# Performance work log

Measured on AMD Instinct MI355X. Metric: run time of the kernel, lower is better.

The kernel has to match this reference:

```python
import jax, jax.numpy as jnp
import numpy as np

DIM, ORDER, HID = 512, 2, 64
B, S = 4, 8192


def setup_inputs() -> dict:
    key = jax.random.key(0)
    ks = jax.random.split(key, 16)
    rnd = lambda k, shape, scale: (jax.random.normal(k, shape, dtype=jnp.float32) * scale)
    return {
        'x': rnd(ks[0], (B, S, DIM), 1.0),
        # ImplicitFilter MLP: Linear(1,64) -> GELU -> Linear(64,64) -> GELU -> Linear(64,dim)
        'w1': rnd(ks[1], (1, HID), 1.0),
        'b1': rnd(ks[2], (HID,), 0.02),
        'w2': rnd(ks[3], (HID, HID), 1.0 / np.sqrt(HID)),
        'b2': rnd(ks[4], (HID,), 0.02),
        'w3': rnd(ks[5], (HID, DIM), 1.0 / np.sqrt(HID)),
        'b3': rnd(ks[6], (DIM,), 0.02),
        # depthwise Conv1d(dim, dim, k=3, padding=1, groups=dim): weight (dim, 3)
        'conv_w': rnd(ks[7], (DIM, 3), 1.0 / np.sqrt(3)),
        'conv_b': rnd(ks[8], (DIM,), 0.02),
        # in_proj: Linear(dim, dim*(order+1))
        'w_in': rnd(ks[9], (DIM, DIM * (ORDER + 1)), 1.0 / np.sqrt(DIM)),
        'b_in': rnd(ks[10], (DIM * (ORDER + 1),), 0.02),
        # out_proj: Linear(dim, dim)
        'w_out': rnd(ks[11], (DIM, DIM), 1.0 / np.sqrt(DIM)),
        'b_out': rnd(ks[12], (DIM,), 0.02),
    }


def _gelu(x):
    return jax.nn.gelu(x, approximate=False)  # torch nn.GELU default is exact erf


def reference(x, w1, b1, w2, b2, w3, b3, conv_w, conv_b, w_in, b_in, w_out, b_out):
    batch, seq_len, dim = x.shape
    # in_proj and split into order+1 paths
    proj = x @ w_in + b_in                      # (B, S, 3D)
    v, u, z = jnp.split(proj, 3, axis=-1)       # each (B, S, D)
    # implicit filter from positions
    pos = jnp.linspace(0.0, 1.0, seq_len, dtype=x.dtype)[:, None]   # (S, 1)
    filt = _gelu(_gelu(pos @ w1 + b1) @ w2 + b2) @ w3 + b3          # (S, D)
    # depthwise short conv, kernel=3, padding=1 (cross-correlation as in torch)
    up = jnp.pad(u, ((0, 0), (1, 1), (0, 0)))
    u_short = (up[:, :-2] * conv_w[:, 0] + up[:, 1:-1] * conv_w[:, 1]
               + up[:, 2:] * conv_w[:, 2] + conv_b)                 # (B, S, D)
    # FFT long convolution (circular, matching torch rfft/irfft with n=seq_len)
    U = jnp.fft.rfft(u_short, axis=1)                               # (B, S//2+1, D)
    F = jnp.fft.rfft(filt, n=seq_len, axis=0)[None]                 # (1, S//2+1, D)
    filtered = jnp.fft.irfft(U * F, n=seq_len, axis=1)              # (B, S, D)
    # multiplicative gates
    out = v * filtered * jax.nn.sigmoid(z)
    return out @ w_out + b_out
```

## Files before the change

### kernel.cpp

```cpp
#include <hip/hip_runtime.h>
#include <math.h>

#define DIM   512
#define NB    4
#define NS    8192
#define FFT_N 8192
#define FT    1024
#define MTOT  (NB*NS)

#define IDX(i) ((i) + ((i) >> 3))
#define XSZ   9216

typedef __attribute__((ext_vector_type(8))) short bf16x8;
typedef __attribute__((ext_vector_type(4))) short short4v;
typedef __attribute__((ext_vector_type(8))) short short8v;
typedef __attribute__((ext_vector_type(4))) float f32x4;

__device__ __forceinline__ float bf2f(unsigned short u) {
    union { unsigned int i; float f; } v; v.i = ((unsigned int)u) << 16; return v.f;
}
__device__ __forceinline__ unsigned short f2bf(float f) {
    union { float f; unsigned int i; } v; v.f = f;
    unsigned int r = v.i + 0x7fffu + ((v.i >> 16) & 1u);
    return (unsigned short)(r >> 16);
}
__device__ __forceinline__ float2 cmulf(float2 a, float2 b) {
    return make_float2(a.x*b.x - a.y*b.y, a.x*b.y + a.y*b.x);
}
__device__ __forceinline__ float2 cadd(float2 a, float2 b) { return make_float2(a.x+b.x, a.y+b.y); }
__device__ __forceinline__ float2 csub(float2 a, float2 b) { return make_float2(a.x-b.x, a.y-b.y); }
__device__ __forceinline__ float gelu_exact(float x) {
    return 0.5f * x * (1.0f + erff(x * 0.70710678118654752f));
}
__device__ __forceinline__ void gload16(const void* g, void* l) {
    __builtin_amdgcn_global_load_lds((const __attribute__((address_space(1))) void*)g,
                                     (__attribute__((address_space(3))) void*)l, 16, 0, 0);
}

__device__ __forceinline__ void castT_body(const float* __restrict__ in,
                                           unsigned short* __restrict__ outT,
                                           int R, int C, int bx, int by, int t,
                                           float tile[64][65]) {
    const int c0 = bx * 64, r0 = by * 64;
    const int rr = t >> 4, c4 = (t & 15) * 4;
    #pragma unroll
    for (int p = 0; p < 4; ++p) {
        const int r = rr + p*16;
        float4 v = *(const float4*)&in[(size_t)(r0 + r)*C + c0 + c4];
        tile[r][c4+0]=v.x; tile[r][c4+1]=v.y; tile[r][c4+2]=v.z; tile[r][c4+3]=v.w;
    }
    __syncthreads();
    const int cc = t >> 4, r4 = (t & 15) * 4;
    #pragma unroll
    for (int p = 0; p < 4; ++p) {
        const int c = cc + p*16;
        short4v o;
        o[0] = (short)f2bf(tile[r4+0][c]); o[1] = (short)f2bf(tile[r4+1][c]);
        o[2] = (short)f2bf(tile[r4+2][c]); o[3] = (short)f2bf(tile[r4+3][c]);
        *(short4v*)&outT[(size_t)(c0 + c)*R + r0 + r4] = o;
    }
}

__global__ void mega_prep_kernel(const float* __restrict__ x, unsigned short* __restrict__ xb,
                                 const float* __restrict__ w_in, unsigned short* __restrict__ w_inT,
                                 const float* __restrict__ w_out, unsigned short* __restrict__ w_outT,
                                 const float* __restrict__ w1, const float* __restrict__ b1,
                                 const float* __restrict__ w2, const float* __restrict__ b2,
                                 const float* __restrict__ w3, const float* __restrict__ b3,
                                 float* __restrict__ filt) {
    __shared__ float tile[64][65];
    __shared__ float h1s[4][64];
    __shared__ float h2s[4][64];
    const int bid = blockIdx.x;
    const int t = threadIdx.x;
    if (bid < 8192) {
        const size_t i = ((size_t)bid * 256 + t) * 8;
        float4 a = *(const float4*)&x[i];
        float4 b = *(const float4*)&x[i+4];
        short8v o;
        o[0]=(short)f2bf(a.x); o[1]=(short)f2bf(a.y); o[2]=(short)f2bf(a.z); o[3]=(short)f2bf(a.w);
        o[4]=(short)f2bf(b.x); o[5]=(short)f2bf(b.y); o[6]=(short)f2bf(b.z); o[7]=(short)f2bf(b.w);
        *(short8v*)&xb[i] = o;
    } else if (bid < 8384) {
        const int li = bid - 8192;
        castT_body(w_in, w_inT, DIM, 1536, li % 24, li / 24, t, tile);
    } else if (bid < 8448) {
        const int li = bid - 8384;
        castT_body(w_out, w_outT, DIM, DIM, li % 8, li / 8, t, tile);
    } else {
        const int sub = t >> 6, lane = t & 63;
        const int s = (bid - 8448) * 4 + sub;
        const float pos = (float)s / (float)(NS - 1);
        h1s[sub][lane] = gelu_exact(pos * w1[lane] + b1[lane]);
        __syncthreads();
        float acc = b2[lane];
        #pragma unroll 8
        for (int j = 0; j < 64; ++j) acc += h1s[sub][j] * w2[j*64 + lane];
        h2s[sub][lane] = gelu_exact(acc);
        __syncthreads();
        for (int d = lane; d < DIM; d += 64) {
            float o = b3[d];
            #pragma unroll 8
            for (int j = 0; j < 64; ++j) o += h2s[sub][j] * w3[j*DIM + d];
            filt[(size_t)s*DIM + d] = o;
        }
    }
}

template<int LOGQ>
__device__ __forceinline__ void dif4_stage(float2* X) {
    const int q = 1 << LOGQ;
    const float step = -6.28318530717958647692f / (float)(4*q);
    #pragma unroll
    for (int it = 0; it < (FFT_N/4)/FT; ++it) {
        const int idx = threadIdx.x + it*FT;
        const int g = idx >> LOGQ, k = idx & (q-1);
        const int base = (g << (LOGQ+2)) + k;
        const int i0 = IDX(base), i1 = IDX(base+q), i2 = IDX(base+2*q), i3 = IDX(base+3*q);
        float2 a=X[i0], b=X[i1], c=X[i2], d=X[i3];
        float2 t0=cadd(a,c), t1=csub(a,c), t2=cadd(b,d), t3=csub(b,d);
        float2 y0=cadd(t0,t2), y2=csub(t0,t2);
        float2 y1=make_float2(t1.x+t3.y, t1.y-t3.x);
        float2 y3=make_float2(t1.x-t3.y, t1.y+t3.x);
        float sv, cv; __sincosf(step*(float)k, &sv, &cv);
        float2 w1=make_float2(cv, sv);
        float2 w2=cmulf(w1, w1);
        float2 w3=cmulf(w2, w1);
        X[i0] = y0;
        X[i1] = cmulf(y1, w1);
        X[i2] = cmulf(y2, w2);
        X[i3] = cmulf(y3, w3);
    }
    __syncthreads();
}

template<int LOGQ>
__device__ __forceinline__ void dit4_stage_inv(float2* X) {
    const int q = 1 << LOGQ;
    const float step = 6.28318530717958647692f / (float)(4*q);
    #pragma unroll
    for (int it = 0; it < (FFT_N/4)/FT; ++it) {
        const int idx = threadIdx.x + it*FT;
        const int g = idx >> LOGQ, k = idx & (q-1);
        const int base = (g << (LOGQ+2)) + k;
        const int i0 = IDX(base), i1 = IDX(base+q), i2 = IDX(base+2*q), i3 = IDX(base+3*q);
        float sv, cv; __sincosf(step*(float)k, &sv, &cv);
        float2 w1=make_float2(cv, sv);
        float2 w2=cmulf(w1, w1);
        float2 w3=cmulf(w2, w1);
        float2 u0=X[i0];
        float2 u1=cmulf(X[i1], w1);
        float2 u2=cmulf(X[i2], w2);
        float2 u3=cmulf(X[i3], w3);
        float2 s02=cadd(u0,u2), d02=csub(u0,u2);
        float2 s13=cadd(u1,u3), d13=csub(u1,u3);
        X[i0] = cadd(s02, s13);
        X[i2] = csub(s02, s13);
        X[i1] = make_float2(d02.x - d13.y, d02.y + d13.x);
        X[i3] = make_float2(d02.x + d13.y, d02.y - d13.x);
    }
    __syncthreads();
}

__device__ __forceinline__ void reg_fwd(float2* E) {
    const float C = 0.70710678118654752f;
    {
        float2 t0=cadd(E[0],E[4]), t1=csub(E[0],E[4]);
        float2 t2=cadd(E[2],E[6]), t3=csub(E[2],E[6]);
        E[0]=cadd(t0,t2);
        E[4]=csub(t0,t2);
        E[2]=make_float2(t1.x+t3.y, t1.y-t3.x);
        E[6]=make_float2(t1.x-t3.y, t1.y+t3.x);
    }
    {
        float2 t0=cadd(E[1],E[5]), t1=csub(E[1],E[5]);
        float2 t2=cadd(E[3],E[7]), t3=csub(E[3],E[7]);
        float2 y0=cadd(t0,t2), y2=csub(t0,t2);
        float2 y1=make_float2(t1.x+t3.y, t1.y-t3.x);
        float2 y3=make_float2(t1.x-t3.y, t1.y+t3.x);
        E[1]=y0;
        E[3]=make_float2(C*(y1.x+y1.y),  C*(y1.y-y1.x));
        E[5]=make_float2(y2.y, -y2.x);
        E[7]=make_float2(C*(y3.y-y3.x), -C*(y3.x+y3.y));
    }
    #pragma unroll
    for (int j = 0; j < 8; j += 2) {
        float2 a=E[j], b=E[j+1];
        E[j]=cadd(a,b); E[j+1]=csub(a,b);
    }
}
__device__ __forceinline__ void reg_inv(float2* E) {
    const float C = 0.70710678118654752f;
    #pragma unroll
    for (int j = 0; j < 8; j += 2) {
        float2 a=E[j], b=E[j+1];
        E[j]=cadd(a,b); E[j+1]=csub(a,b);
    }
    {
        float2 u0=E[0], u1=E[2], u2=E[4], u3=E[6];
        float2 s02=cadd(u0,u2), d02=csub(u0,u2);
        float2 s13=cadd(u1,u3), d13=csub(u1,u3);
        E[0]=cadd(s02,s13);
        E[4]=csub(s02,s13);
        E[2]=make_float2(d02.x - d13.y, d02.y + d13.x);
        E[6]=make_float2(d02.x + d13.y, d02.y - d13.x);
    }
    {
        float2 z1=E[3], z2=E[5], z3=E[7];
        float2 u0=E[1];
        float2 u1=make_float2(C*(z1.x - z1.y), C*(z1.x + z1.y));
        float2 u2=make_float2(-z2.y, z2.x);
        float2 u3=make_float2(-C*(z3.x + z3.y), C*(z3.x - z3.y));
        float2 s02=cadd(u0,u2), d02=csub(u0,u2);
        float2 s13=cadd(u1,u3), d13=csub(u1,u3);
        E[1]=cadd(s02,s13);
        E[5]=csub(s02,s13);
        E[3]=make_float2(d02.x - d13.y, d02.y + d13.x);
        E[7]=make_float2(d02.x + d13.y, d02.y - d13.x);
    }
}

__device__ __forceinline__ void load8p(const float2* X, int t, float2* E) {
    const float2* b = X + 9*t;
    #pragma unroll
    for (int j = 0; j < 8; ++j) E[j] = b[j];
}
__device__ __forceinline__ void store8p(float2* X, int t, const float2* E) {
    float2* b = X + 9*t;
    #pragma unroll
    for (int j = 0; j < 8; ++j) b[j] = E[j];
}

__global__ __launch_bounds__(FT)
void filtconv_kernel(const float* __restrict__ filtT, float2* __restrict__ Fbr,
                     const unsigned short* __restrict__ u,
                     const float* __restrict__ conv_w, const float* __restrict__ conv_b,
                     unsigned short* __restrict__ uT) {
    __shared__ __align__(16) char fsm[XSZ * sizeof(float2)];
    const int bid = blockIdx.x;
    const int t = threadIdx.x;
    if (bid < 512) {
        float2* X = (float2*)fsm;
        const int dd = bid;
        const float* f = filtT + (size_t)dd * FFT_N;
        {
            float4 a = *(const float4*)(f + 8*t);
            float4 b = *(const float4*)(f + 8*t + 4);
            float2 E[8];
            E[0]=make_float2(a.x,0.f); E[1]=make_float2(a.y,0.f);
            E[2]=make_float2(a.z,0.f); E[3]=make_float2(a.w,0.f);
            E[4]=make_float2(b.x,0.f); E[5]=make_float2(b.y,0.f);
            E[6]=make_float2(b.z,0.f); E[7]=make_float2(b.w,0.f);
            store8p(X, t, E);
        }
        __syncthreads();
        dif4_stage<11>(X);
        dif4_stage<9>(X);
        dif4_stage<7>(X);
        dif4_stage<5>(X);
        dif4_stage<3>(X);
        {
            float2 E[8];
            load8p(X, t, E);
            reg_fwd(E);
            float2* o = Fbr + (size_t)dd*FFT_N + 8*t;
            #pragma unroll
            for (int j = 0; j < 8; ++j) o[j] = E[j];
        }
    } else {
        float (*tile)[65] = (float(*)[65])fsm;
        const int lb = bid - 512;
        const int dt = lb & 7, st = (lb >> 3) & 127, b = lb >> 10;
        const int d0 = dt*64, s0 = st*64;
        const int rr = t >> 4, c4 = (t & 15) * 4;
        for (int r = rr; r < 66; r += 64) {
            const int s = s0 + r - 1;
            float v0=0.f, v1=0.f, v2=0.f, v3=0.f;
            if (s >= 0 && s < NS) {
                short4v xv = *(const short4v*)&u[((size_t)(b*NS + s))*DIM + d0 + c4];
                v0=bf2f((unsigned short)xv[0]); v1=bf2f((unsigned short)xv[1]);
                v2=bf2f((unsigned short)xv[2]); v3=bf2f((unsigned short)xv[3]);
            }
            tile[r][c4]=v0; tile[r][c4+1]=v1; tile[r][c4+2]=v2; tile[r][c4+3]=v3;
        }
        __syncthreads();
        const int dc = t >> 4, s4 = (t & 15) * 4;
        const int d = d0 + dc;
        const float w0 = conv_w[d*3], w1 = conv_w[d*3+1], w2 = conv_w[d*3+2];
        const float cb = conv_b[d];
        short4v o;
        #pragma unroll
        for (int j = 0; j < 4; ++j) {
            const int sx = s4 + j;
            const float val = tile[sx][dc]*w0 + tile[sx+1][dc]*w1 + tile[sx+2][dc]*w2 + cb;
            o[j] = (short)f2bf(val);
        }
        *(short4v*)&uT[((size_t)(b*DIM + d))*FFT_N + s0 + s4] = o;
    }
}

__global__ __launch_bounds__(FT)
void fft_conv_kernel(unsigned short* __restrict__ uT, const float2* __restrict__ Fbr) {
    __shared__ float2 X[XSZ];
    const int d = blockIdx.x & (DIM - 1);
    const int p = blockIdx.x >> 9;
    unsigned short* u1 = uT + (size_t)((2*p    )*DIM + d) * FFT_N;
    unsigned short* u2 = uT + (size_t)((2*p + 1)*DIM + d) * FFT_N;
    const int t = threadIdx.x;
    {
        short8v a = *(const short8v*)(u1 + 8*t);
        short8v b = *(const short8v*)(u2 + 8*t);
        float2 E[8];
        #pragma unroll
        for (int j = 0; j < 8; ++j)
            E[j] = make_float2(bf2f((unsigned short)a[j]), bf2f((unsigned short)b[j]));
        store8p(X, t, E);
    }
    __syncthreads();
    dif4_stage<11>(X);
    dif4_stage<9>(X);
    dif4_stage<7>(X);
    dif4_stage<5>(X);
    dif4_stage<3>(X);
    {
        float2 E[8];
        load8p(X, t, E);
        reg_fwd(E);
        const float2* F = Fbr + (size_t)d*FFT_N + 8*t;
        #pragma unroll
        for (int j = 0; j < 8; ++j) E[j] = cmulf(E[j], F[j]);
        reg_inv(E);
        store8p(X, t, E);
    }
    __syncthreads();
    dit4_stage_inv<3>(X);
    dit4_stage_inv<5>(X);
    dit4_stage_inv<7>(X);
    dit4_stage_inv<9>(X);
    dit4_stage_inv<11>(X);
    {
        float2 E[8];
        load8p(X, t, E);
        const float sc = 1.0f / (float)FFT_N;
        short8v a, b;
        #pragma unroll
        for (int j = 0; j < 8; ++j) {
            a[j] = (short)f2bf(E[j].x * sc);
            b[j] = (short)f2bf(E[j].y * sc);
        }
        *(short8v*)(u1 + 8*t) = a;
        *(short8v*)(u2 + 8*t) = b;
    }
}

__global__ void gate_kernel(unsigned short* __restrict__ vg, const unsigned short* __restrict__ yT) {
    __shared__ float tile[64][65];
    const int bid = blockIdx.x;
    const int dt = bid & 7, st = (bid >> 3) & 127, b = bid >> 10;
    const int d0 = dt*64, s0 = st*64;
    const int t = threadIdx.x;
    const int dl = t >> 4, s4 = (t & 15) * 4;
    #pragma unroll
    for (int p = 0; p < 4; ++p) {
        const int d = dl + p*16;
        short4v y = *(const short4v*)&yT[((size_t)(b*DIM + d0 + d))*FFT_N + s0 + s4];
        tile[d][s4]  =bf2f((unsigned short)y[0]); tile[d][s4+1]=bf2f((unsigned short)y[1]);
        tile[d][s4+2]=bf2f((unsigned short)y[2]); tile[d][s4+3]=bf2f((unsigned short)y[3]);
    }
    __syncthreads();
    const int sl = t >> 4, d4 = (t & 15) * 4;
    #pragma unroll
    for (int p = 0; p < 4; ++p) {
        const int s = s0 + sl + p*16;
        unsigned short* pv = &vg[((size_t)(b*NS + s))*DIM + d0 + d4];
        short4v v = *(short4v*)pv;
        short4v o;
        #pragma unroll
        for (int j = 0; j < 4; ++j)
            o[j] = (short)f2bf(bf2f((unsigned short)v[j]) * tile[d4+j][sl + p*16]);
        *(short4v*)pv = o;
    }
}

template<int MODE>
__global__ __launch_bounds__(256)
void gemm_bt_kernel(const unsigned short* __restrict__ A,
                    const unsigned short* __restrict__ BT,
                    const float* __restrict__ bias,
                    float* __restrict__ Cf,
                    unsigned short* __restrict__ Cb) {
    __shared__ unsigned short As[2][4096];
    __shared__ unsigned short Bs[2][4096];
    const int tid = threadIdx.x;
    const int wid = tid >> 6, lane = tid & 63;
    const int bid = blockIdx.y * 4 + blockIdx.x;
    const int swz = (bid & 7) * 128 + (bid >> 3);
    const int m0 = (swz >> 2) * 128, n0 = (swz & 3) * 128;
    const int srow = wid*16 + (lane >> 2);
    const int scol = (lane & 3) * 8;
    const unsigned short* gA = A  + (size_t)(m0 + srow)*DIM + scol;
    const unsigned short* gB = BT + (size_t)(n0 + srow)*DIM + scol;
    const int wr = wid >> 1, wc = wid & 1;
    const int fr = lane & 15, fq = lane >> 4;
    f32x4 acc[4][4] = {};
    gload16(gA,                  &As[0][wid*512]);
    gload16(gA + (size_t)64*DIM, &As[0][wid*512 + 2048]);
    gload16(gB,                  &Bs[0][wid*512]);
    gload16(gB + (size_t)64*DIM, &Bs[0][wid*512 + 2048]);
    int cur = 0;
    for (int k0 = 0; k0 < DIM; k0 += 32) {
        __syncthreads();
        if (k0 + 32 < DIM) {
            const int nx = cur ^ 1;
            gload16(gA + k0 + 32,                  &As[nx][wid*512]);
            gload16(gA + k0 + 32 + (size_t)64*DIM, &As[nx][wid*512 + 2048]);
            gload16(gB + k0 + 32,                  &Bs[nx][wid*512]);
            gload16(gB + k0 + 32 + (size_t)64*DIM, &Bs[nx][wid*512 + 2048]);
        }
        bf16x8 af[4], bfr[4];
        #pragma unroll
        for (int mi = 0; mi < 4; ++mi)
            af[mi] = *(const bf16x8*)&As[cur][(wr*64 + mi*16 + fr)*32 + fq*8];
        #pragma unroll
        for (int ni = 0; ni < 4; ++ni)
            bfr[ni] = *(const bf16x8*)&Bs[cur][(wc*64 + ni*16 + fr)*32 + fq*8];
        #pragma unroll
        for (int mi = 0; mi < 4; ++mi)
            #pragma unroll
            for (int ni = 0; ni < 4; ++ni)
                acc[mi][ni] = __builtin_amdgcn_mfma_f32_16x16x32_bf16(af[mi], bfr[ni], acc[mi][ni], 0, 0, 0);
        cur ^= 1;
    }
    #pragma unroll
    for (int ni = 0; ni < 4; ++ni) {
        const int c = n0 + wc*64 + ni*16 + fr;
        const float bv = bias[c];
        #pragma unroll
        for (int mi = 0; mi < 4; ++mi) {
            const int rbase = m0 + wr*64 + mi*16 + fq*4;
            #pragma unroll
            for (int j = 0; j < 4; ++j) {
                const size_t idx = (size_t)(rbase + j)*DIM + c;
                const float val = acc[mi][ni][j] + bv;
                if (MODE == 0) Cb[idx] = f2bf(val);
                else           Cf[idx] = val;
            }
        }
    }
}

__global__ __launch_bounds__(256)
void gemm_vzu2t_kernel(const unsigned short* __restrict__ A,
                       const unsigned short* __restrict__ BT,
                       const float* __restrict__ bias,
                       unsigned short* __restrict__ Gb,
                       unsigned short* __restrict__ Ub,
                       const float* __restrict__ filt,
                       float* __restrict__ filtT) {
    __shared__ __align__(16) char gsm[49152];
    unsigned short (*As)[4096] = (unsigned short(*)[4096])(gsm);
    unsigned short (*B1)[4096] = (unsigned short(*)[4096])(gsm + 16384);
    unsigned short (*B2)[4096] = (unsigned short(*)[4096])(gsm + 32768);
    const int tid = threadIdx.x;
    const int wid = tid >> 6, lane = tid & 63;
    const int bid = blockIdx.y * 4 + blockIdx.x;

    if (bid >= 2048) {
        float (*tile)[65] = (float(*)[65])gsm;
        const int li = bid - 2048;
        const int c0 = (li & 7) * 64, r0 = (li >> 3) * 64;
        const int rr = tid >> 4, c4 = (tid & 15) * 4;
        #pragma unroll
        for (int p = 0; p < 4; ++p) {
            const int r = rr + p*16;
            float4 v = *(const float4*)&filt[(size_t)(r0 + r)*DIM + c0 + c4];
            tile[r][c4+0]=v.x; tile[r][c4+1]=v.y; tile[r][c4+2]=v.z; tile[r][c4+3]=v.w;
        }
        __syncthreads();
        const int cc = tid >> 4, r4 = (tid & 15) * 4;
        #pragma unroll
        for (int p = 0; p < 4; ++p) {
            const int c = cc + p*16;
            float4 o = make_float4(tile[r4+0][c], tile[r4+1][c], tile[r4+2][c], tile[r4+3][c]);
            *(float4*)&filtT[(size_t)(c0 + c)*NS + r0 + r4] = o;
        }
        return;
    }

    const bool is_u = bid >= 1024;
    const int lbid = bid & 1023;
    const int swz = (lbid & 7) * 128 + (lbid >> 3);
    const int m0 = (swz >> 2) * 128, n0 = (swz & 3) * 128;
    const int srow = wid*16 + (lane >> 2);
    const int scol = (lane & 3) * 8;
    const unsigned short* gA = A + (size_t)(m0 + srow)*DIM + scol;
    const int wr = wid >> 1, wc = wid & 1;
    const int fr = lane & 15, fq = lane >> 4;

    if (!is_u) {
        const unsigned short* gBv = BT + (size_t)(n0 + srow)*DIM + scol;
        const unsigned short* gBz = BT + (size_t)(1024 + n0 + srow)*DIM + scol;
        f32x4 accv[4][4] = {};
        f32x4 accz[4][4] = {};
        gload16(gA,                   &As[0][wid*512]);
        gload16(gA  + (size_t)64*DIM, &As[0][wid*512 + 2048]);
        gload16(gBv,                  &B1[0][wid*512]);
        gload16(gBv + (size_t)64*DIM, &B1[0][wid*512 + 2048]);
        gload16(gBz,                  &B2[0][wid*512]);
        gload16(gBz + (size_t)64*DIM, &B2[0][wid*512 + 2048]);
        int cur = 0;
        for (int k0 = 0; k0 < DIM; k0 += 32) {
            __syncthreads();
            if (k0 + 32 < DIM) {
                const int nx = cur ^ 1;
                gload16(gA  + k0 + 32,                  &As[nx][wid*512]);
                gload16(gA  + k0 + 32 + (size_t)64*DIM, &As[nx][wid*512 + 2048]);
                gload16(gBv + k0 + 32,                  &B1[nx][wid*512]);
                gload16(gBv + k0 + 32 + (size_t)64*DIM, &B1[nx][wid*512 + 2048]);
                gload16(gBz + k0 + 32,                  &B2[nx][wid*512]);
                gload16(gBz + k0 + 32 + (size_t)64*DIM, &B2[nx][wid*512 + 2048]);
            }
            bf16x8 af[4], bf_[4];
            #pragma unroll
            for (int mi = 0; mi < 4; ++mi)
                af[mi] = *(const bf16x8*)&As[cur][(wr*64 + mi*16 + fr)*32 + fq*8];
            #pragma unroll
            for (int ni = 0; ni < 4; ++ni)
                bf_[ni] = *(const bf16x8*)&B1[cur][(wc*64 + ni*16 + fr)*32 + fq*8];
            #pragma unroll
            for (int mi = 0; mi < 4; ++mi)
                #pragma unroll
                for (int ni = 0; ni < 4; ++ni)
                    accv[mi][ni] = __builtin_amdgcn_mfma_f32_16x16x32_bf16(af[mi], bf_[ni], accv[mi][ni], 0, 0, 0);
            #pragma unroll
            for (int ni = 0; ni < 4; ++ni)
                bf_[ni] = *(const bf16x8*)&B2[cur][(wc*64 + ni*16 + fr)*32 + fq*8];
            #pragma unroll
            for (int mi = 0; mi < 4; ++mi)
                #pragma unroll
                for (int ni = 0; ni < 4; ++ni)
                    accz[mi][ni] = __builtin_amdgcn_mfma_f32_16x16x32_bf16(af[mi], bf_[ni], accz[mi][ni], 0, 0, 0);
            cur ^= 1;
        }
        #pragma unroll
        for (int ni = 0; ni < 4; ++ni) {
            const int c = n0 + wc*64 + ni*16 + fr;
            const float bv = bias[c];
            const float bz = bias[1024 + c];
            #pragma unroll
            for (int mi = 0; mi < 4; ++mi) {
                const int rbase = m0 + wr*64 + mi*16 + fq*4;
                #pragma unroll
                for (int j = 0; j < 4; ++j) {
                    const size_t idx = (size_t)(rbase + j)*DIM + c;
                    const float vv = accv[mi][ni][j] + bv;
                    const float zz = accz[mi][ni][j] + bz;
                    const float sg = 1.0f / (1.0f + __expf(-zz));
                    Gb[idx] = f2bf(vv * sg);
                }
            }
        }
    } else {
        const unsigned short* gBu = BT + (size_t)(512 + n0 + srow)*DIM + scol;
        f32x4 acc[4][4] = {};
        gload16(gA,                   &As[0][wid*512]);
        gload16(gA  + (size_t)64*DIM, &As[0][wid*512 + 2048]);
        gload16(gBu,                  &B1[0][wid*512]);
        gload16(gBu + (size_t)64*DIM, &B1[0][wid*512 + 2048]);
        int cur = 0;
        for (int k0 = 0; k0 < DIM; k0 += 32) {
            __syncthreads();
            if (k0 + 32 < DIM) {
                const int nx = cur ^ 1;
                gload16(gA  + k0 + 32,                  &As[nx][wid*512]);
                gload16(gA  + k0 + 32 + (size_t)64*DIM, &As[nx][wid*512 + 2048]);
                gload16(gBu + k0 + 32,                  &B1[nx][wid*512]);
                gload16(gBu + k0 + 32 + (size_t)64*DIM, &B1[nx][wid*512 + 2048]);
            }
            bf16x8 af[4], bf_[4];
            #pragma unroll
            for (int mi = 0; mi < 4; ++mi)
                af[mi] = *(const bf16x8*)&As[cur][(wr*64 + mi*16 + fr)*32 + fq*8];
            #pragma unroll
            for (int ni = 0; ni < 4; ++ni)
                bf_[ni] = *(const bf16x8*)&B1[cur][(wc*64 + ni*16 + fr)*32 + fq*8];
            #pragma unroll
            for (int mi = 0; mi < 4; ++mi)
                #pragma unroll
                for (int ni = 0; ni < 4; ++ni)
                    acc[mi][ni] = __builtin_amdgcn_mfma_f32_16x16x32_bf16(af[mi], bf_[ni], acc[mi][ni], 0, 0, 0);
            cur ^= 1;
        }
        #pragma unroll
        for (int ni = 0; ni < 4; ++ni) {
            const int c = n0 + wc*64 + ni*16 + fr;
            const float bu = bias[512 + c];
            #pragma unroll
            for (int mi = 0; mi < 4; ++mi) {
                const int rbase = m0 + wr*64 + mi*16 + fq*4;
                #pragma unroll
                for (int j = 0; j < 4; ++j) {
                    const size_t idx = (size_t)(rbase + j)*DIM + c;
                    Ub[idx] = f2bf(acc[mi][ni][j] + bu);
                }
            }
        }
    }
}

extern "C" void kernel_launch(void* const* d_in, const int* in_sizes, int n_in,
                              void* d_out, int out_size, void* d_ws, size_t ws_size,
                              hipStream_t stream) {
    const float* x      = (const float*)d_in[0];
    const float* w1     = (const float*)d_in[1];
    const float* b1     = (const float*)d_in[2];
    const float* w2     = (const float*)d_in[3];
    const float* b2     = (const float*)d_in[4];
    const float* w3     = (const float*)d_in[5];
    const float* b3     = (const float*)d_in[6];
    const float* conv_w = (const float*)d_in[7];
    const float* conv_b = (const float*)d_in[8];
    const float* w_in   = (const float*)d_in[9];
    const float* b_in   = (const float*)d_in[10];
    const float* w_out  = (const float*)d_in[11];
    const float* b_out  = (const float*)d_in[12];
    float* out = (float*)d_out;

    const size_t NEED = 167772160ULL;
    if (ws_size < NEED) return;
    char* ws = (char*)d_ws;
    float2*         Fbr    = (float2*)ws;
    float*          filt   = (float*)ws;
    unsigned short* xb     = (unsigned short*)(ws + (size_t)( 32<<20));
    unsigned short* W2     = (unsigned short*)(ws + (size_t)( 64<<20));
    unsigned short* W3     = (unsigned short*)(ws + (size_t)( 96<<20));
    char*           W4     = ws + (size_t)(128<<20);
    unsigned short* w_inT  = (unsigned short*)W4;
    unsigned short* w_outT = (unsigned short*)(W4 + (size_t)(2<<20));
    float*          filtT  = (float*)(W4 + (size_t)(4<<20));

    mega_prep_kernel<<<10496, 256, 0, stream>>>(x, xb, w_in, w_inT, w_out, w_outT,
                                                w1, b1, w2, b2, w3, b3, filt);
    gemm_vzu2t_kernel<<<dim3(4, 768), 256, 0, stream>>>(xb, w_inT, b_in, W2, W3, filt, filtT);
    filtconv_kernel<<<4608, FT, 0, stream>>>(filtT, Fbr, W3, conv_w, conv_b, xb);
    fft_conv_kernel<<<(NB/2)*DIM, FT, 0, stream>>>(xb, Fbr);
    gate_kernel<<<NB*(NS/64)*(DIM/64), 256, 0, stream>>>(W2, xb);
    gemm_bt_kernel<2><<<dim3(4, MTOT/128), 256, 0, stream>>>(W2, w_outT, b_out, out, nullptr);
}
```

Before: 257.4 us.

## Write u transposed from GEMM epilogue and fuse short conv into FFT load

The u-projection GEMM epilogue now stages its tile in shared memory and writes u directly in a (batch, dim, seq) transposed layout. The depthwise kernel-3 short convolution moves into the FFT kernel's load phase, using neighbour loads at the 8-element chunk edges. This drops the separate transpose-plus-conv pass and one full round trip of u through global memory. In exchange the GEMM epilogue gains two barriers and an LDS transpose, and the FFT kernel issues extra scalar halo loads.

Measured after the change: 247.0 us. 1.04x faster.

```diff
diff --git a/kernel.cpp b/kernel.cpp
--- a/kernel.cpp
+++ b/kernel.cpp
@@ -232,75 +232,40 @@
 }
 
 __global__ __launch_bounds__(FT)
-void filtconv_kernel(const float* __restrict__ filtT, float2* __restrict__ Fbr,
-                     const unsigned short* __restrict__ u,
-                     const float* __restrict__ conv_w, const float* __restrict__ conv_b,
-                     unsigned short* __restrict__ uT) {
-    __shared__ __align__(16) char fsm[XSZ * sizeof(float2)];
-    const int bid = blockIdx.x;
+void fft_filt_kernel(const float* __restrict__ filtT, float2* __restrict__ Fbr) {
+    __shared__ float2 X[XSZ];
+    const int dd = blockIdx.x;
     const int t = threadIdx.x;
-    if (bid < 512) {
-        float2* X = (float2*)fsm;
-        const int dd = bid;
-        const float* f = filtT + (size_t)dd * FFT_N;
-        {
-            float4 a = *(const float4*)(f + 8*t);
-            float4 b = *(const float4*)(f + 8*t + 4);
-            float2 E[8];
-            E[0]=make_float2(a.x,0.f); E[1]=make_float2(a.y,0.f);
-            E[2]=make_float2(a.z,0.f); E[3]=make_float2(a.w,0.f);
-            E[4]=make_float2(b.x,0.f); E[5]=make_float2(b.y,0.f);
-            E[6]=make_float2(b.z,0.f); E[7]=make_float2(b.w,0.f);
-            store8p(X, t, E);
-        }
-        __syncthreads();
-        dif4_stage<11>(X);
-        dif4_stage<9>(X);
-        dif4_stage<7>(X);
-        dif4_stage<5>(X);
-        dif4_stage<3>(X);
-        {
-            float2 E[8];
-            load8p(X, t, E);
-            reg_fwd(E);
-            float2* o = Fbr + (size_t)dd*FFT_N + 8*t;
-            #pragma unroll
-            for (int j = 0; j < 8; ++j) o[j] = E[j];
-        }
-    } else {
-        float (*tile)[65] = (float(*)[65])fsm;
-        const int lb = bid - 512;
-        const int dt = lb & 7, st = (lb >> 3) & 127, b = lb >> 10;
-        const int d0 = dt*64, s0 = st*64;
-        const int rr = t >> 4, c4 = (t & 15) * 4;
-        for (int r = rr; r < 66; r += 64) {
-            const int s = s0 + r - 1;
-            float v0=0.f, v1=0.f, v2=0.f, v3=0.f;
-            if (s >= 0 && s < NS) {
-                short4v xv = *(const short4v*)&u[((size_t)(b*NS + s))*DIM + d0 + c4];
-                v0=bf2f((unsigned short)xv[0]); v1=bf2f((unsigned short)xv[1]);
-                v2=bf2f((unsigned short)xv[2]); v3=bf2f((unsigned short)xv[3]);
-            }
-            tile[r][c4]=v0; tile[r][c4+1]=v1; tile[r][c4+2]=v2; tile[r][c4+3]=v3;
-        }
-        __syncthreads();
-        const int dc = t >> 4, s4 = (t & 15) * 4;
-        const int d = d0 + dc;
-        const float w0 = conv_w[d*3], w1 = conv_w[d*3+1], w2 = conv_w[d*3+2];
-        const float cb = conv_b[d];
-        short4v o;
-        #pragma unroll
-        for (int j = 0; j < 4; ++j) {
-            const int sx = s4 + j;
-            const float val = tile[sx][dc]*w0 + tile[sx+1][dc]*w1 + tile[sx+2][dc]*w2 + cb;
-            o[j] = (short)f2bf(val);
-        }
-        *(short4v*)&uT[((size_t)(b*DIM + d))*FFT_N + s0 + s4] = o;
+    const float* f = filtT + (size_t)dd * FFT_N;
+    {
+        float4 a = *(const float4*)(f + 8*t);
+        float4 b = *(const float4*)(f + 8*t + 4);
+        float2 E[8];
+        E[0]=make_float2(a.x,0.f); E[1]=make_float2(a.y,0.f);
+        E[2]=make_float2(a.z,0.f); E[3]=make_float2(a.w,0.f);
+        E[4]=make_float2(b.x,0.f); E[5]=make_float2(b.y,0.f);
+        E[6]=make_float2(b.z,0.f); E[7]=make_float2(b.w,0.f);
+        store8p(X, t, E);
+    }
+    __syncthreads();
+    dif4_stage<11>(X);
+    dif4_stage<9>(X);
+    dif4_stage<7>(X);
+    dif4_stage<5>(X);
+    dif4_stage<3>(X);
+    {
+        float2 E[8];
+        load8p(X, t, E);
+        reg_fwd(E);
+        float2* o = Fbr + (size_t)dd*FFT_N + 8*t;
+        #pragma unroll
+        for (int j = 0; j < 8; ++j) o[j] = E[j];
     }
 }
 
 __global__ __launch_bounds__(FT)
-void fft_conv_kernel(unsigned short* __restrict__ uT, const float2* __restrict__ Fbr) {
+void fft_conv_kernel(unsigned short* __restrict__ uT, const float2* __restrict__ Fbr,
+                     const float* __restrict__ conv_w, const float* __restrict__ conv_b) {
     __shared__ float2 X[XSZ];
     const int d = blockIdx.x & (DIM - 1);
     const int p = blockIdx.x >> 9;
@@ -310,10 +275,25 @@
     {
         short8v a = *(const short8v*)(u1 + 8*t);
         short8v b = *(const short8v*)(u2 + 8*t);
+        const float al = (t == 0)    ? 0.f : bf2f(u1[8*t - 1]);
+        const float ar = (t == FT-1) ? 0.f : bf2f(u1[8*t + 8]);
+        const float bl = (t == 0)    ? 0.f : bf2f(u2[8*t - 1]);
+        const float br = (t == FT-1) ? 0.f : bf2f(u2[8*t + 8]);
+        const float w0 = conv_w[d*3], w1 = conv_w[d*3+1], w2c = conv_w[d*3+2];
+        const float cb = conv_b[d];
+        float xa[10], xb[10];
+        xa[0] = al; xb[0] = bl;
+        #pragma unroll
+        for (int j = 0; j < 8; ++j) {
+            xa[j+1] = bf2f((unsigned short)a[j]);
+            xb[j+1] = bf2f((unsigned short)b[j]);
+        }
+        xa[9] = ar; xb[9] = br;
         float2 E[8];
         #pragma unroll
         for (int j = 0; j < 8; ++j)
-            E[j] = make_float2(bf2f((unsigned short)a[j]), bf2f((unsigned short)b[j]));
+            E[j] = make_float2(w0*xa[j] + w1*xa[j+1] + w2c*xa[j+2] + cb,
+                               w0*xb[j] + w1*xb[j+1] + w2c*xb[j+2] + cb);
         store8p(X, t, E);
     }
     __syncthreads();
@@ -454,7 +434,7 @@
                        const unsigned short* __restrict__ BT,
                        const float* __restrict__ bias,
                        unsigned short* __restrict__ Gb,
-                       unsigned short* __restrict__ Ub,
+                       unsigned short* __restrict__ UbT,
                        const float* __restrict__ filt,
                        float* __restrict__ filtT) {
     __shared__ __align__(16) char gsm[49152];
@@ -591,20 +571,30 @@
                     acc[mi][ni] = __builtin_amdgcn_mfma_f32_16x16x32_bf16(af[mi], bf_[ni], acc[mi][ni], 0, 0, 0);
             cur ^= 1;
         }
+        __syncthreads();
+        unsigned short (*tileT)[136] = (unsigned short(*)[136])gsm;
         #pragma unroll
         for (int ni = 0; ni < 4; ++ni) {
-            const int c = n0 + wc*64 + ni*16 + fr;
-            const float bu = bias[512 + c];
+            const int dl = wc*64 + ni*16 + fr;
+            const float bu = bias[512 + n0 + dl];
             #pragma unroll
             for (int mi = 0; mi < 4; ++mi) {
-                const int rbase = m0 + wr*64 + mi*16 + fq*4;
+                const int slb = wr*64 + mi*16 + fq*4;
                 #pragma unroll
-                for (int j = 0; j < 4; ++j) {
-                    const size_t idx = (size_t)(rbase + j)*DIM + c;
-                    Ub[idx] = f2bf(acc[mi][ni][j] + bu);
-                }
+                for (int j = 0; j < 4; ++j)
+                    tileT[dl][slb + j] = f2bf(acc[mi][ni][j] + bu);
             }
         }
+        __syncthreads();
+        const int b   = m0 >> 13;
+        const int s0m = m0 & (NS - 1);
+        const int row  = tid >> 1;
+        const int half = (tid & 1) * 64;
+        unsigned short* dst = UbT + ((size_t)(b*DIM + n0 + row))*NS + s0m + half;
+        const unsigned short* srcT = &tileT[row][half];
+        #pragma unroll
+        for (int i = 0; i < 8; ++i)
+            *(short8v*)(dst + i*8) = *(const short8v*)(srcT + i*8);
     }
 }
 
@@ -642,8 +632,8 @@
     mega_prep_kernel<<<10496, 256, 0, stream>>>(x, xb, w_in, w_inT, w_out, w_outT,
                                                 w1, b1, w2, b2, w3, b3, filt);
     gemm_vzu2t_kernel<<<dim3(4, 768), 256, 0, stream>>>(xb, w_inT, b_in, W2, W3, filt, filtT);
-    filtconv_kernel<<<4608, FT, 0, stream>>>(filtT, Fbr, W3, conv_w, conv_b, xb);
-    fft_conv_kernel<<<(NB/2)*DIM, FT, 0, stream>>>(xb, Fbr);
-    gate_kernel<<<NB*(NS/64)*(DIM/64), 256, 0, stream>>>(W2, xb);
+    fft_filt_kernel<<<DIM, FT, 0, stream>>>(filtT, Fbr);
+    fft_conv_kernel<<<(NB/2)*DIM, FT, 0, stream>>>(W3, Fbr, conv_w, conv_b);
+    gate_kernel<<<NB*(NS/64)*(DIM/64), 256, 0, stream>>>(W2, W3);
     gemm_bt_kernel<2><<<dim3(4, MTOT/128), 256, 0, stream>>>(W2, w_outT, b_out, out, nullptr);
 }
```
